# Performance work log

Hardware: AMD Instinct MI355X
Metric: run time of the kernel (lower is better)

Reference implementation:

```python
import jax, jax.numpy as jnp
import numpy as np

B, T, C_IN, C_HID, C_EMB, K, MAX_DUR = 16, 512, 512, 256, 384, 5, 8
MAX_MEL = T * MAX_DUR  # static upper bound on regulated length (4096)
LRELU_SLOPE = 0.3
PAD = (K - 1) // 2
EPS = 1e-5


def setup_inputs() -> dict:
    key = jax.random.key(0)
    ks = jax.random.split(key, 14)
    s = 0.05
    return {
        "x": jax.random.normal(ks[0], (B, T, C_IN), jnp.float32),
        "x_res": jax.random.normal(ks[1], (B, T, C_IN), jnp.float32),
        "duration_target": jax.random.randint(ks[2], (B, T), 0, MAX_DUR, dtype=jnp.int32),
        "embeddings": jax.random.normal(ks[3], (B, T, C_EMB), jnp.float32),
        "src_mask": jnp.zeros((B, T), jnp.bool_),
        "conv1_w": s * jax.random.normal(ks[4], (K, C_IN, C_HID), jnp.float32),
        "conv1_b": jnp.zeros((C_HID,), jnp.float32),
        "ln1_g": jnp.ones((C_HID,), jnp.float32),
        "ln1_b": jnp.zeros((C_HID,), jnp.float32),
        "conv2_w": s * jax.random.normal(ks[5], (K, C_HID, C_HID), jnp.float32),
        "conv2_b": jnp.zeros((C_HID,), jnp.float32),
        "ln2_g": jnp.ones((C_HID,), jnp.float32),
        "ln2_b": jnp.zeros((C_HID,), jnp.float32),
        "lin_w": s * jax.random.normal(ks[6], (C_HID, 1), jnp.float32),
        "lin_b": jnp.zeros((1,), jnp.float32),
    }


def _conv1d(x, w, b):
    # x: [B, T, Cin], w: [K, Cin, Cout] -> [B, T, Cout] (same padding)
    y = jax.lax.conv_general_dilated(
        x, w, window_strides=(1,), padding=[(PAD, PAD)],
        dimension_numbers=("NWC", "WIO", "NWC"))
    return y + b


def _layer_norm(x, g, b):
    mu = jnp.mean(x, axis=-1, keepdims=True)
    var = jnp.mean(jnp.square(x - mu), axis=-1, keepdims=True)
    return (x - mu) * jax.lax.rsqrt(var + EPS) * g + b


def _duration_predictor(x, mask, c1w, c1b, g1, b1, c2w, c2b, g2, b2, lw, lb):
    h = jax.nn.leaky_relu(_conv1d(x, c1w, c1b), LRELU_SLOPE)
    h = _layer_norm(h, g1, b1)  # dropout is identity at eval
    h = jax.nn.leaky_relu(_conv1d(h, c2w, c2b), LRELU_SLOPE)
    h = _layer_norm(h, g2, b2)
    h = (h @ lw + lb).squeeze(-1)  # [B, T]
    return jnp.where(mask, 0.0, h)


def _length_regulate(x, duration):
    # Fused prefix-sum + gather replacement for the looped expand/cat/pad.
    # token i occupies output frames [cumsum[i-1], cumsum[i])
    cum = jnp.cumsum(duration, axis=1)              # [B, T]
    total = cum[:, -1]                              # [B] mel lengths
    pos = jnp.arange(MAX_MEL, dtype=cum.dtype)      # [MAX_MEL]
    idx = jax.vmap(lambda c: jnp.searchsorted(c, pos, side="right"))(cum)  # [B, MAX_MEL]
    idx = jnp.clip(idx, 0, duration.shape[1] - 1)
    valid = (pos[None, :] < total[:, None])         # [B, MAX_MEL]
    out = jnp.take_along_axis(x, idx[..., None], axis=1)
    out = out * valid[..., None].astype(x.dtype)    # zero-padded past mel_len
    return out, total.astype(jnp.int32)


def reference(x, x_res, duration_target, embeddings, src_mask,
              conv1_w, conv1_b, ln1_g, ln1_b, conv2_w, conv2_b, ln2_g, ln2_b,
              lin_w, lin_b):
    # upsample_train path: x_res is detached before the duration predictor
    x_res = jax.lax.stop_gradient(x_res)
    log_duration_prediction = _duration_predictor(
        x_res, src_mask, conv1_w, conv1_b, ln1_g, ln1_b,
        conv2_w, conv2_b, ln2_g, ln2_b, lin_w, lin_b)
    x_up, _ = _length_regulate(x, duration_target)
    emb_up, _ = _length_regulate(embeddings, duration_target)
    return x_up, log_duration_prediction, emb_up
```

## Files before the change

### kernel.cpp

```cpp
#include <hip/hip_runtime.h>


constexpr int Bn = 16, Tn = 512, CIN1 = 512, CHID = 256, CEMB = 384, MAXMEL = 4096;
constexpr int NROWS = Bn * Tn;
#define LRELU 0.3f
#define EPSV 1e-5f

typedef __attribute__((ext_vector_type(8))) short bf16x8;
typedef __attribute__((ext_vector_type(4))) float f32x4;
typedef unsigned short ushort_t;

static __device__ __forceinline__ ushort_t f2bf(float f) {
  unsigned u = __builtin_bit_cast(unsigned, f);
  unsigned r = (u + 0x7fffu + ((u >> 16) & 1u)) >> 16;
  return (ushort_t)r;
}
static __device__ __forceinline__ float bf2f(ushort_t h) {
  unsigned u = ((unsigned)h) << 16;
  return __builtin_bit_cast(float, u);
}

__global__ __launch_bounds__(256) void wprep_kernel(const float* __restrict__ w,
                                                    ushort_t* __restrict__ hi,
                                                    ushort_t* __restrict__ lo,
                                                    int CI) {
  const int gid = blockIdx.x * 256 + threadIdx.x;
  const int ksh = gid / (CI * 256);
  const int rem = gid - ksh * CI * 256;
  const int ci = rem >> 8, co = rem & 255;
  const float v = w[gid];
  const ushort_t h = f2bf(v);
  const int ci32 = ci >> 5, cob = co >> 4;
  const int l = ((ci >> 3) & 3) * 16 + (co & 15);
  const int j = ci & 7;
  const size_t dst = ((size_t)((ksh * (CI / 32) + ci32) * 16 + cob)) * 512 + l * 8 + j;
  hi[dst] = h;
  lo[dst] = f2bf(v - bf2f(h));
}

template <int CI, bool F32IN>
__global__ __launch_bounds__(512, 4) void conv_mfma_kernel(
    const float* __restrict__ xin,
    const ushort_t* __restrict__ inhi,
    const ushort_t* __restrict__ wBhi,
    const ushort_t* __restrict__ wBlo,
    float* __restrict__ part) {
  constexpr int CIQ = CI / 4;
  constexpr int NCHUNK = CIQ / 64;
  constexpr int ROWS = 132, LDSTRIDE = 72;
  __shared__ ushort_t sAhi[ROWS * LDSTRIDE];
  __shared__ ushort_t sAlo[F32IN ? ROWS * LDSTRIDE : 1];

  const int mt = blockIdx.x, ns = blockIdx.y, ks = blockIdx.z;
  const int b = mt >> 2, t0 = (mt & 3) * 128;
  const int tid = threadIdx.x;
  const int l = tid & 63, w = tid >> 6;
  const int mh = w >> 1, nh = w & 1;
  const int lm = l & 15, lq = l >> 4;

  f32x4 acc[2][4];
#pragma unroll
  for (int im = 0; im < 2; ++im)
#pragma unroll
    for (int jn = 0; jn < 4; ++jn) acc[im][jn] = (f32x4){0.f, 0.f, 0.f, 0.f};

  const ushort_t* pBh = wBhi + l * 8;
  const ushort_t* pBl = wBlo + l * 8;
  const int cobBase = ns * 8 + nh * 4;
  const int rowBase = mh * 32 + lm;

#pragma unroll 1
  for (int chunk = 0; chunk < NCHUNK; ++chunk) {
    {
      const int cibase = ks * CIQ + chunk * 64;
#pragma unroll 1
      for (int i = 0; i < 9; ++i) {
        const int p = i * 512 + tid;
        if (p < ROWS * 32) {
          const int r = p >> 5, c2 = (p & 31) * 2;
          const int t = t0 - 2 + r;
          unsigned hv = 0, lv = 0;
          if ((unsigned)t < (unsigned)Tn) {
            const size_t src = (size_t)(b * Tn + t) * CI + cibase + c2;
            if (F32IN) {
              const float2 v = *(const float2*)(xin + src);
              const ushort_t h0 = f2bf(v.x), h1 = f2bf(v.y);
              hv = (unsigned)h0 | ((unsigned)h1 << 16);
              lv = (unsigned)f2bf(v.x - bf2f(h0)) |
                   ((unsigned)f2bf(v.y - bf2f(h1)) << 16);
            } else {
              hv = *(const unsigned*)(inhi + src);
            }
          }
          *(unsigned*)&sAhi[r * LDSTRIDE + c2] = hv;
          if (F32IN) *(unsigned*)&sAlo[r * LDSTRIDE + c2] = lv;
        }
      }
    }
    __syncthreads();

#pragma unroll 1
    for (int ksh = 0; ksh < 5; ++ksh) {
#pragma unroll
      for (int kk = 0; kk < 2; ++kk) {
        bf16x8 a_h[2], a_l[2];
#pragma unroll
        for (int im = 0; im < 2; ++im) {
          const int ad = (rowBase + im * 16 + ksh) * LDSTRIDE + kk * 32 + lq * 8;
          a_h[im] = *(const bf16x8*)&sAhi[ad];
          if (F32IN) a_l[im] = *(const bf16x8*)&sAlo[ad];
        }
        const int ci32 = ks * (CIQ / 32) + chunk * 2 + kk;
        const int frBase = (ksh * (CI / 32) + ci32) * 16 + cobBase;
#pragma unroll
        for (int jn = 0; jn < 4; ++jn) {
          const size_t fo = (size_t)(frBase + jn) * 512;
          const bf16x8 bh = *(const bf16x8*)(pBh + fo);
          const bf16x8 bl = *(const bf16x8*)(pBl + fo);
#pragma unroll
          for (int im = 0; im < 2; ++im) {
            acc[im][jn] = __builtin_amdgcn_mfma_f32_16x16x32_bf16(a_h[im], bh, acc[im][jn], 0, 0, 0);
            if (F32IN)
              acc[im][jn] = __builtin_amdgcn_mfma_f32_16x16x32_bf16(a_l[im], bh, acc[im][jn], 0, 0, 0);
            acc[im][jn] = __builtin_amdgcn_mfma_f32_16x16x32_bf16(a_h[im], bl, acc[im][jn], 0, 0, 0);
          }
        }
      }
    }
    __syncthreads();
  }

  float* pOut = part + (size_t)ks * NROWS * 256;
#pragma unroll
  for (int im = 0; im < 2; ++im)
#pragma unroll
    for (int jn = 0; jn < 4; ++jn) {
      const int col = ns * 128 + nh * 64 + jn * 16 + lm;
#pragma unroll
      for (int reg = 0; reg < 4; ++reg) {
        const int grow = b * Tn + t0 + mh * 32 + im * 16 + lq * 4 + reg;
        pOut[(size_t)grow * 256 + col] = acc[im][jn][reg];
      }
    }
}

template <bool FINAL>
__global__ __launch_bounds__(256) void ln_kernel(
    const float* __restrict__ part,
    const float* __restrict__ bias, const float* __restrict__ g,
    const float* __restrict__ be, ushort_t* __restrict__ h1,
    const float* __restrict__ lw, const float* __restrict__ lb,
    const unsigned char* __restrict__ mask, float* __restrict__ ldp) {
  const int row = blockIdx.x * 4 + (threadIdx.x >> 6);
  const int l = threadIdx.x & 63;
  const float4 bi = ((const float4*)bias)[l];
  float v0 = bi.x, v1 = bi.y, v2 = bi.z, v3 = bi.w;
#pragma unroll
  for (int k = 0; k < 4; ++k) {
    const float4 p = ((const float4*)(part + (size_t)k * NROWS * 256))[row * 64 + l];
    v0 += p.x; v1 += p.y; v2 += p.z; v3 += p.w;
  }
  v0 = (v0 > 0.f) ? v0 : LRELU * v0;
  v1 = (v1 > 0.f) ? v1 : LRELU * v1;
  v2 = (v2 > 0.f) ? v2 : LRELU * v2;
  v3 = (v3 > 0.f) ? v3 : LRELU * v3;
  float s = v0 + v1 + v2 + v3;
  float s2 = v0 * v0 + v1 * v1 + v2 * v2 + v3 * v3;
#pragma unroll
  for (int off = 32; off >= 1; off >>= 1) {
    s += __shfl_xor(s, off);
    s2 += __shfl_xor(s2, off);
  }
  const float mu = s * (1.f / 256.f);
  const float var = s2 * (1.f / 256.f) - mu * mu;
  const float rs = rsqrtf(var + EPSV);
  const float4 gg = ((const float4*)g)[l];
  const float4 bb = ((const float4*)be)[l];
  const float h0 = (v0 - mu) * rs * gg.x + bb.x;
  const float h1v = (v1 - mu) * rs * gg.y + bb.y;
  const float h2 = (v2 - mu) * rs * gg.z + bb.z;
  const float h3 = (v3 - mu) * rs * gg.w + bb.w;
  if (!FINAL) {
    ushort4 uh;
    uh.x = f2bf(h0); uh.y = f2bf(h1v); uh.z = f2bf(h2); uh.w = f2bf(h3);
    ((ushort4*)h1)[row * 64 + l] = uh;
  } else {
    const float4 lv = ((const float4*)lw)[l];
    float d = h0 * lv.x + h1v * lv.y + h2 * lv.z + h3 * lv.w;
#pragma unroll
    for (int off = 32; off >= 1; off >>= 1) d += __shfl_xor(d, off);
    if (l == 0) {
      float val = d + lb[0];
      if (mask[row]) val = 0.f;
      ldp[row] = val;
    }
  }
}

__global__ __launch_bounds__(512) void build_idx_kernel(const int* __restrict__ dur,
                                                        int* __restrict__ idx) {
  __shared__ int cum[Tn];
  const int b = blockIdx.x, t = threadIdx.x;
  const int d = dur[b * Tn + t];
  cum[t] = d;
  __syncthreads();
  for (int off = 1; off < Tn; off <<= 1) {
    int v = (t >= off) ? cum[t - off] : 0;
    __syncthreads();
    cum[t] += v;
    __syncthreads();
  }
  const int end = cum[t];
  for (int p = end - d; p < end; ++p) idx[b * MAXMEL + p] = t;
  const int total = cum[Tn - 1];
  for (int p = total + t; p < MAXMEL; p += Tn) idx[b * MAXMEL + p] = -1;
}

__global__ __launch_bounds__(256) void gather_kernel(const float* __restrict__ x,
                                                     const float* __restrict__ emb,
                                                     const int* __restrict__ idx,
                                                     float* __restrict__ x_up,
                                                     float* __restrict__ emb_up) {
  const float4* x4 = (const float4*)x;
  const float4* e4 = (const float4*)emb;
  float4* xu4 = (float4*)x_up;
  float4* eu4 = (float4*)emb_up;
  const int tid0 = blockIdx.x * 256 + threadIdx.x;
  const int stride = gridDim.x * 256;
  const float4 z = make_float4(0.f, 0.f, 0.f, 0.f);
  for (int u = tid0; u < Bn * MAXMEL * 128; u += stride) {
    const int bp = u >> 7, i = u & 127;
    const int t = idx[bp];
    const int b = bp >> 12;
    xu4[u] = (t >= 0) ? x4[((b << 9) + t) * 128 + i] : z;
  }
  for (int u = tid0; u < Bn * MAXMEL * 96; u += stride) {
    const int bp = u / 96, i = u - bp * 96;
    const int t = idx[bp];
    const int b = bp >> 12;
    eu4[u] = (t >= 0) ? e4[((b << 9) + t) * 96 + i] : z;
  }
}

extern "C" void kernel_launch(void* const* d_in, const int* in_sizes, int n_in,
                              void* d_out, int out_size, void* d_ws, size_t ws_size,
                              hipStream_t stream) {
  const float* x     = (const float*)d_in[0];
  const float* x_res = (const float*)d_in[1];
  const int*   dur   = (const int*)d_in[2];
  const float* emb   = (const float*)d_in[3];
  const unsigned char* mask = (const unsigned char*)d_in[4];
  const float* c1w = (const float*)d_in[5];
  const float* c1b = (const float*)d_in[6];
  const float* g1  = (const float*)d_in[7];
  const float* b1  = (const float*)d_in[8];
  const float* c2w = (const float*)d_in[9];
  const float* c2b = (const float*)d_in[10];
  const float* g2  = (const float*)d_in[11];
  const float* b2  = (const float*)d_in[12];
  const float* lw  = (const float*)d_in[13];
  const float* lb  = (const float*)d_in[14];

  float* x_up   = (float*)d_out;
  float* ldp    = x_up + (size_t)Bn * MAXMEL * CIN1;
  float* emb_up = ldp + (size_t)Bn * Tn;

  float* part = emb_up;
  ushort_t* w1hi = (ushort_t*)(part + (size_t)4 * NROWS * 256);
  ushort_t* w1lo = w1hi + (size_t)5 * 512 * 256;
  ushort_t* w2hi = w1lo + (size_t)5 * 512 * 256;
  ushort_t* w2lo = w2hi + (size_t)5 * 256 * 256;

  int* idx = (int*)d_ws;
  ushort_t* h1 = (ushort_t*)((char*)d_ws + (size_t)Bn * MAXMEL * sizeof(int));

  wprep_kernel<<<5 * 512 * 256 / 256, 256, 0, stream>>>(c1w, w1hi, w1lo, 512);
  wprep_kernel<<<5 * 256 * 256 / 256, 256, 0, stream>>>(c2w, w2hi, w2lo, 256);
  conv_mfma_kernel<512, true><<<dim3(64, 2, 4), 512, 0, stream>>>(
      x_res, nullptr, w1hi, w1lo, part);
  ln_kernel<false><<<NROWS / 4, 256, 0, stream>>>(
      part, c1b, g1, b1, h1, nullptr, nullptr, nullptr, nullptr);
  conv_mfma_kernel<256, false><<<dim3(64, 2, 4), 512, 0, stream>>>(
      nullptr, h1, w2hi, w2lo, part);
  ln_kernel<true><<<NROWS / 4, 256, 0, stream>>>(
      part, c2b, g2, b2, nullptr, lw, lb, mask, ldp);
  build_idx_kernel<<<Bn, Tn, 0, stream>>>(dur, idx);
  gather_kernel<<<2048, 256, 0, stream>>>(x, emb, idx, x_up, emb_up);
}
```

Baseline: 408.5 us.

## Fuse conv with LayerNorm, drop split-bf16 precision, use nontemporal gather stores

Drops the hi/lo bf16 split so each conv needs one MFMA per fragment instead of two or three. LayerNorm and LeakyReLU are fused into the conv kernel through an LDS tile, which removes the split-K partial buffer and the separate LN kernels. Tiles shrink to 32 rows by full 256 columns per block, and the gather stores become nontemporal. The plain-bf16 path risks accuracy relative to the fp32 reference, and the 256-block grid may leave much of the GPU idle during the convs.

Result: no change. 413.6 us (+1.2%).

```diff
diff --git a/kernel.cpp b/kernel.cpp
--- a/kernel.cpp
+++ b/kernel.cpp
@@ -15,47 +15,42 @@
   unsigned r = (u + 0x7fffu + ((u >> 16) & 1u)) >> 16;
   return (ushort_t)r;
 }
-static __device__ __forceinline__ float bf2f(ushort_t h) {
-  unsigned u = ((unsigned)h) << 16;
-  return __builtin_bit_cast(float, u);
-}
 
 __global__ __launch_bounds__(256) void wprep_kernel(const float* __restrict__ w,
                                                     ushort_t* __restrict__ hi,
-                                                    ushort_t* __restrict__ lo,
                                                     int CI) {
   const int gid = blockIdx.x * 256 + threadIdx.x;
   const int ksh = gid / (CI * 256);
   const int rem = gid - ksh * CI * 256;
   const int ci = rem >> 8, co = rem & 255;
-  const float v = w[gid];
-  const ushort_t h = f2bf(v);
   const int ci32 = ci >> 5, cob = co >> 4;
   const int l = ((ci >> 3) & 3) * 16 + (co & 15);
   const int j = ci & 7;
   const size_t dst = ((size_t)((ksh * (CI / 32) + ci32) * 16 + cob)) * 512 + l * 8 + j;
-  hi[dst] = h;
-  lo[dst] = f2bf(v - bf2f(h));
+  hi[dst] = f2bf(w[gid]);
 }
 
 template <int CI, bool F32IN>
-__global__ __launch_bounds__(512, 4) void conv_mfma_kernel(
+__global__ __launch_bounds__(256, 2) void conv_ln_mfma_kernel(
     const float* __restrict__ xin,
-    const ushort_t* __restrict__ inhi,
-    const ushort_t* __restrict__ wBhi,
-    const ushort_t* __restrict__ wBlo,
-    float* __restrict__ part) {
-  constexpr int CIQ = CI / 4;
-  constexpr int NCHUNK = CIQ / 64;
-  constexpr int ROWS = 132, LDSTRIDE = 72;
-  __shared__ ushort_t sAhi[ROWS * LDSTRIDE];
-  __shared__ ushort_t sAlo[F32IN ? ROWS * LDSTRIDE : 1];
-
-  const int mt = blockIdx.x, ns = blockIdx.y, ks = blockIdx.z;
-  const int b = mt >> 2, t0 = (mt & 3) * 128;
+    const ushort_t* __restrict__ inbf,
+    const ushort_t* __restrict__ wB,
+    const float* __restrict__ bias, const float* __restrict__ g,
+    const float* __restrict__ be,
+    ushort_t* __restrict__ h1out,
+    const float* __restrict__ lw, const float* __restrict__ lb,
+    const unsigned char* __restrict__ mask, float* __restrict__ ldp) {
+  constexpr bool FINAL = !F32IN;
+  constexpr int NCHUNK = CI / 64;
+  constexpr int LDSTRIDE = 72;
+  __shared__ ushort_t sA[36 * LDSTRIDE];
+  __shared__ float sC[32 * 260];
+  __shared__ float sps[32 * 8], spq[32 * 8];
+  __shared__ float smu[32], srs[32];
+
+  const int b = blockIdx.x >> 4, t0 = (blockIdx.x & 15) * 32;
   const int tid = threadIdx.x;
-  const int l = tid & 63, w = tid >> 6;
-  const int mh = w >> 1, nh = w & 1;
+  const int l = tid & 63, nh = tid >> 6;
   const int lm = l & 15, lq = l >> 4;
 
   f32x4 acc[2][4];
@@ -64,36 +59,29 @@
 #pragma unroll
     for (int jn = 0; jn < 4; ++jn) acc[im][jn] = (f32x4){0.f, 0.f, 0.f, 0.f};
 
-  const ushort_t* pBh = wBhi + l * 8;
-  const ushort_t* pBl = wBlo + l * 8;
-  const int cobBase = ns * 8 + nh * 4;
-  const int rowBase = mh * 32 + lm;
+  const ushort_t* pB = wB + l * 8;
 
 #pragma unroll 1
   for (int chunk = 0; chunk < NCHUNK; ++chunk) {
     {
-      const int cibase = ks * CIQ + chunk * 64;
+      const int cibase = chunk * 64;
 #pragma unroll 1
-      for (int i = 0; i < 9; ++i) {
-        const int p = i * 512 + tid;
-        if (p < ROWS * 32) {
+      for (int i = 0; i < 5; ++i) {
+        const int p = i * 256 + tid;
+        if (p < 36 * 32) {
           const int r = p >> 5, c2 = (p & 31) * 2;
           const int t = t0 - 2 + r;
-          unsigned hv = 0, lv = 0;
+          unsigned hv = 0;
           if ((unsigned)t < (unsigned)Tn) {
             const size_t src = (size_t)(b * Tn + t) * CI + cibase + c2;
             if (F32IN) {
               const float2 v = *(const float2*)(xin + src);
-              const ushort_t h0 = f2bf(v.x), h1 = f2bf(v.y);
-              hv = (unsigned)h0 | ((unsigned)h1 << 16);
-              lv = (unsigned)f2bf(v.x - bf2f(h0)) |
-                   ((unsigned)f2bf(v.y - bf2f(h1)) << 16);
+              hv = (unsigned)f2bf(v.x) | ((unsigned)f2bf(v.y) << 16);
             } else {
-              hv = *(const unsigned*)(inhi + src);
+              hv = *(const unsigned*)(inbf + src);
             }
           }
-          *(unsigned*)&sAhi[r * LDSTRIDE + c2] = hv;
-          if (F32IN) *(unsigned*)&sAlo[r * LDSTRIDE + c2] = lv;
+          *(unsigned*)&sA[r * LDSTRIDE + c2] = hv;
         }
       }
     }
@@ -103,96 +91,104 @@
     for (int ksh = 0; ksh < 5; ++ksh) {
 #pragma unroll
       for (int kk = 0; kk < 2; ++kk) {
-        bf16x8 a_h[2], a_l[2];
-#pragma unroll
-        for (int im = 0; im < 2; ++im) {
-          const int ad = (rowBase + im * 16 + ksh) * LDSTRIDE + kk * 32 + lq * 8;
-          a_h[im] = *(const bf16x8*)&sAhi[ad];
-          if (F32IN) a_l[im] = *(const bf16x8*)&sAlo[ad];
-        }
-        const int ci32 = ks * (CIQ / 32) + chunk * 2 + kk;
-        const int frBase = (ksh * (CI / 32) + ci32) * 16 + cobBase;
+        bf16x8 a[2];
+#pragma unroll
+        for (int im = 0; im < 2; ++im)
+          a[im] = *(const bf16x8*)&sA[(im * 16 + lm + ksh) * LDSTRIDE + kk * 32 + lq * 8];
+        const int frBase = (ksh * (CI / 32) + chunk * 2 + kk) * 16 + nh * 4;
 #pragma unroll
         for (int jn = 0; jn < 4; ++jn) {
-          const size_t fo = (size_t)(frBase + jn) * 512;
-          const bf16x8 bh = *(const bf16x8*)(pBh + fo);
-          const bf16x8 bl = *(const bf16x8*)(pBl + fo);
-#pragma unroll
-          for (int im = 0; im < 2; ++im) {
-            acc[im][jn] = __builtin_amdgcn_mfma_f32_16x16x32_bf16(a_h[im], bh, acc[im][jn], 0, 0, 0);
-            if (F32IN)
-              acc[im][jn] = __builtin_amdgcn_mfma_f32_16x16x32_bf16(a_l[im], bh, acc[im][jn], 0, 0, 0);
-            acc[im][jn] = __builtin_amdgcn_mfma_f32_16x16x32_bf16(a_h[im], bl, acc[im][jn], 0, 0, 0);
-          }
+          const bf16x8 bv = *(const bf16x8*)(pB + (size_t)(frBase + jn) * 512);
+#pragma unroll
+          for (int im = 0; im < 2; ++im)
+            acc[im][jn] = __builtin_amdgcn_mfma_f32_16x16x32_bf16(a[im], bv, acc[im][jn], 0, 0, 0);
         }
       }
     }
     __syncthreads();
   }
 
-  float* pOut = part + (size_t)ks * NROWS * 256;
 #pragma unroll
   for (int im = 0; im < 2; ++im)
 #pragma unroll
     for (int jn = 0; jn < 4; ++jn) {
-      const int col = ns * 128 + nh * 64 + jn * 16 + lm;
-#pragma unroll
-      for (int reg = 0; reg < 4; ++reg) {
-        const int grow = b * Tn + t0 + mh * 32 + im * 16 + lq * 4 + reg;
-        pOut[(size_t)grow * 256 + col] = acc[im][jn][reg];
-      }
-    }
-}
-
-template <bool FINAL>
-__global__ __launch_bounds__(256) void ln_kernel(
-    const float* __restrict__ part,
-    const float* __restrict__ bias, const float* __restrict__ g,
-    const float* __restrict__ be, ushort_t* __restrict__ h1,
-    const float* __restrict__ lw, const float* __restrict__ lb,
-    const unsigned char* __restrict__ mask, float* __restrict__ ldp) {
-  const int row = blockIdx.x * 4 + (threadIdx.x >> 6);
-  const int l = threadIdx.x & 63;
-  const float4 bi = ((const float4*)bias)[l];
-  float v0 = bi.x, v1 = bi.y, v2 = bi.z, v3 = bi.w;
-#pragma unroll
-  for (int k = 0; k < 4; ++k) {
-    const float4 p = ((const float4*)(part + (size_t)k * NROWS * 256))[row * 64 + l];
-    v0 += p.x; v1 += p.y; v2 += p.z; v3 += p.w;
-  }
-  v0 = (v0 > 0.f) ? v0 : LRELU * v0;
-  v1 = (v1 > 0.f) ? v1 : LRELU * v1;
-  v2 = (v2 > 0.f) ? v2 : LRELU * v2;
-  v3 = (v3 > 0.f) ? v3 : LRELU * v3;
-  float s = v0 + v1 + v2 + v3;
-  float s2 = v0 * v0 + v1 * v1 + v2 * v2 + v3 * v3;
-#pragma unroll
-  for (int off = 32; off >= 1; off >>= 1) {
-    s += __shfl_xor(s, off);
-    s2 += __shfl_xor(s2, off);
-  }
-  const float mu = s * (1.f / 256.f);
-  const float var = s2 * (1.f / 256.f) - mu * mu;
-  const float rs = rsqrtf(var + EPSV);
-  const float4 gg = ((const float4*)g)[l];
-  const float4 bb = ((const float4*)be)[l];
-  const float h0 = (v0 - mu) * rs * gg.x + bb.x;
-  const float h1v = (v1 - mu) * rs * gg.y + bb.y;
-  const float h2 = (v2 - mu) * rs * gg.z + bb.z;
-  const float h3 = (v3 - mu) * rs * gg.w + bb.w;
+      const int col = nh * 64 + jn * 16 + lm;
+#pragma unroll
+      for (int reg = 0; reg < 4; ++reg)
+        sC[(im * 16 + lq * 4 + reg) * 260 + col] = acc[im][jn][reg];
+    }
+  __syncthreads();
+
+  const int row = tid >> 3, sg = tid & 7;
+  float v[32];
+  float s = 0.f, s2 = 0.f;
+#pragma unroll
+  for (int q = 0; q < 8; ++q) {
+    const f32x4 c4 = *(const f32x4*)&sC[row * 260 + sg * 32 + q * 4];
+    const f32x4 b4 = ((const f32x4*)bias)[sg * 8 + q];
+    float x0 = c4.x + b4.x, x1 = c4.y + b4.y, x2 = c4.z + b4.z, x3 = c4.w + b4.w;
+    x0 = (x0 > 0.f) ? x0 : LRELU * x0;
+    x1 = (x1 > 0.f) ? x1 : LRELU * x1;
+    x2 = (x2 > 0.f) ? x2 : LRELU * x2;
+    x3 = (x3 > 0.f) ? x3 : LRELU * x3;
+    v[q * 4] = x0; v[q * 4 + 1] = x1; v[q * 4 + 2] = x2; v[q * 4 + 3] = x3;
+    s += x0 + x1 + x2 + x3;
+    s2 += x0 * x0 + x1 * x1 + x2 * x2 + x3 * x3;
+  }
+  sps[row * 8 + sg] = s;
+  spq[row * 8 + sg] = s2;
+  __syncthreads();
+  if (tid < 32) {
+    float ts = 0.f, tq = 0.f;
+#pragma unroll
+    for (int q = 0; q < 8; ++q) { ts += sps[tid * 8 + q]; tq += spq[tid * 8 + q]; }
+    const float mu = ts * (1.f / 256.f);
+    const float var = tq * (1.f / 256.f) - mu * mu;
+    smu[tid] = mu;
+    srs[tid] = rsqrtf(var + EPSV);
+  }
+  __syncthreads();
+  const float mu = smu[row], rs = srs[row];
+  const int rowg = b * Tn + t0 + row;
+
   if (!FINAL) {
-    ushort4 uh;
-    uh.x = f2bf(h0); uh.y = f2bf(h1v); uh.z = f2bf(h2); uh.w = f2bf(h3);
-    ((ushort4*)h1)[row * 64 + l] = uh;
+    unsigned up[16];
+#pragma unroll
+    for (int q = 0; q < 8; ++q) {
+      const f32x4 g4 = ((const f32x4*)g)[sg * 8 + q];
+      const f32x4 e4 = ((const f32x4*)be)[sg * 8 + q];
+      const float h0 = (v[q * 4] - mu) * rs * g4.x + e4.x;
+      const float h1 = (v[q * 4 + 1] - mu) * rs * g4.y + e4.y;
+      const float h2 = (v[q * 4 + 2] - mu) * rs * g4.z + e4.z;
+      const float h3 = (v[q * 4 + 3] - mu) * rs * g4.w + e4.w;
+      up[q * 2] = (unsigned)f2bf(h0) | ((unsigned)f2bf(h1) << 16);
+      up[q * 2 + 1] = (unsigned)f2bf(h2) | ((unsigned)f2bf(h3) << 16);
+    }
+    uint4* dst = (uint4*)(h1out + (size_t)rowg * 256 + sg * 32);
+#pragma unroll
+    for (int q = 0; q < 4; ++q)
+      dst[q] = make_uint4(up[q * 4], up[q * 4 + 1], up[q * 4 + 2], up[q * 4 + 3]);
   } else {
-    const float4 lv = ((const float4*)lw)[l];
-    float d = h0 * lv.x + h1v * lv.y + h2 * lv.z + h3 * lv.w;
-#pragma unroll
-    for (int off = 32; off >= 1; off >>= 1) d += __shfl_xor(d, off);
-    if (l == 0) {
-      float val = d + lb[0];
-      if (mask[row]) val = 0.f;
-      ldp[row] = val;
+    float d = 0.f;
+#pragma unroll
+    for (int q = 0; q < 8; ++q) {
+      const f32x4 g4 = ((const f32x4*)g)[sg * 8 + q];
+      const f32x4 e4 = ((const f32x4*)be)[sg * 8 + q];
+      const f32x4 l4 = ((const f32x4*)lw)[sg * 8 + q];
+      d += ((v[q * 4] - mu) * rs * g4.x + e4.x) * l4.x;
+      d += ((v[q * 4 + 1] - mu) * rs * g4.y + e4.y) * l4.y;
+      d += ((v[q * 4 + 2] - mu) * rs * g4.z + e4.z) * l4.z;
+      d += ((v[q * 4 + 3] - mu) * rs * g4.w + e4.w) * l4.w;
+    }
+    sps[row * 8 + sg] = d;
+    __syncthreads();
+    if (tid < 32) {
+      float td = 0.f;
+#pragma unroll
+      for (int q = 0; q < 8; ++q) td += sps[tid * 8 + q];
+      float val = td + lb[0];
+      if (mask[b * Tn + t0 + tid]) val = 0.f;
+      ldp[b * Tn + t0 + tid] = val;
     }
   }
 }
@@ -221,24 +217,26 @@
                                                      const int* __restrict__ idx,
                                                      float* __restrict__ x_up,
                                                      float* __restrict__ emb_up) {
-  const float4* x4 = (const float4*)x;
-  const float4* e4 = (const float4*)emb;
-  float4* xu4 = (float4*)x_up;
-  float4* eu4 = (float4*)emb_up;
+  const f32x4* x4 = (const f32x4*)x;
+  const f32x4* e4 = (const f32x4*)emb;
+  f32x4* xu4 = (f32x4*)x_up;
+  f32x4* eu4 = (f32x4*)emb_up;
   const int tid0 = blockIdx.x * 256 + threadIdx.x;
   const int stride = gridDim.x * 256;
-  const float4 z = make_float4(0.f, 0.f, 0.f, 0.f);
+  const f32x4 z = (f32x4){0.f, 0.f, 0.f, 0.f};
   for (int u = tid0; u < Bn * MAXMEL * 128; u += stride) {
     const int bp = u >> 7, i = u & 127;
     const int t = idx[bp];
     const int b = bp >> 12;
-    xu4[u] = (t >= 0) ? x4[((b << 9) + t) * 128 + i] : z;
+    const f32x4 v = (t >= 0) ? x4[((b << 9) + t) * 128 + i] : z;
+    __builtin_nontemporal_store(v, &xu4[u]);
   }
   for (int u = tid0; u < Bn * MAXMEL * 96; u += stride) {
     const int bp = u / 96, i = u - bp * 96;
     const int t = idx[bp];
     const int b = bp >> 12;
-    eu4[u] = (t >= 0) ? e4[((b << 9) + t) * 96 + i] : z;
+    const f32x4 v = (t >= 0) ? e4[((b << 9) + t) * 96 + i] : z;
+    __builtin_nontemporal_store(v, &eu4[u]);
   }
 }
 
@@ -265,25 +263,17 @@
   float* ldp    = x_up + (size_t)Bn * MAXMEL * CIN1;
   float* emb_up = ldp + (size_t)Bn * Tn;
 
-  float* part = emb_up;
-  ushort_t* w1hi = (ushort_t*)(part + (size_t)4 * NROWS * 256);
-  ushort_t* w1lo = w1hi + (size_t)5 * 512 * 256;
-  ushort_t* w2hi = w1lo + (size_t)5 * 512 * 256;
-  ushort_t* w2lo = w2hi + (size_t)5 * 256 * 256;
-
   int* idx = (int*)d_ws;
-  ushort_t* h1 = (ushort_t*)((char*)d_ws + (size_t)Bn * MAXMEL * sizeof(int));
-
-  wprep_kernel<<<5 * 512 * 256 / 256, 256, 0, stream>>>(c1w, w1hi, w1lo, 512);
-  wprep_kernel<<<5 * 256 * 256 / 256, 256, 0, stream>>>(c2w, w2hi, w2lo, 256);
-  conv_mfma_kernel<512, true><<<dim3(64, 2, 4), 512, 0, stream>>>(
-      x_res, nullptr, w1hi, w1lo, part);
-  ln_kernel<false><<<NROWS / 4, 256, 0, stream>>>(
-      part, c1b, g1, b1, h1, nullptr, nullptr, nullptr, nullptr);
-  conv_mfma_kernel<256, false><<<dim3(64, 2, 4), 512, 0, stream>>>(
-      nullptr, h1, w2hi, w2lo, part);
-  ln_kernel<true><<<NROWS / 4, 256, 0, stream>>>(
-      part, c2b, g2, b2, nullptr, lw, lb, mask, ldp);
+  ushort_t* h1 = (ushort_t*)((char*)d_ws + (size_t)Bn * MAXMEL * 4);
+  ushort_t* w1 = h1 + (size_t)NROWS * 256;
+  ushort_t* w2 = w1 + (size_t)5 * 512 * 256;
+
+  wprep_kernel<<<5 * 512 * 256 / 256, 256, 0, stream>>>(c1w, w1, 512);
+  wprep_kernel<<<5 * 256 * 256 / 256, 256, 0, stream>>>(c2w, w2, 256);
   build_idx_kernel<<<Bn, Tn, 0, stream>>>(dur, idx);
+  conv_ln_mfma_kernel<512, true><<<256, 256, 0, stream>>>(
+      x_res, nullptr, w1, c1b, g1, b1, h1, nullptr, nullptr, nullptr, nullptr);
+  conv_ln_mfma_kernel<256, false><<<256, 256, 0, stream>>>(
+      nullptr, h1, w2, c2b, g2, b2, nullptr, lw, lb, mask, ldp);
   gather_kernel<<<2048, 256, 0, stream>>>(x, emb, idx, x_up, emb_up);
 }
```

## Drop split-bf16 conv precision, use 32x32 MFMA tiles without split-K, nontemporal gather stores

Applied to the files above, without the earlier changes.

The conv kernels no longer emulate fp32 with hi/lo bf16 pairs. They use a single bf16 pass with 32x32x16 MFMA, smaller 32-row tiles, no split-K partial buffers, and a swizzled LDS layout. The LayerNorm kernels now read one raw buffer instead of summing four partials. The gather writes use nontemporal stores, and build_idx is launched earlier. This cuts MFMA count and partial-sum traffic, but drops accuracy from roughly fp32 to plain bf16, which may break the tolerance.

After: 371.2 us. -9.1%, faster.

```diff
diff --git a/kernel.cpp b/kernel.cpp
--- a/kernel.cpp
+++ b/kernel.cpp
@@ -8,6 +8,7 @@
 
 typedef __attribute__((ext_vector_type(8))) short bf16x8;
 typedef __attribute__((ext_vector_type(4))) float f32x4;
+typedef __attribute__((ext_vector_type(16))) float f32x16;
 typedef unsigned short ushort_t;
 
 static __device__ __forceinline__ ushort_t f2bf(float f) {
@@ -15,85 +16,66 @@
   unsigned r = (u + 0x7fffu + ((u >> 16) & 1u)) >> 16;
   return (ushort_t)r;
 }
-static __device__ __forceinline__ float bf2f(ushort_t h) {
-  unsigned u = ((unsigned)h) << 16;
-  return __builtin_bit_cast(float, u);
-}
 
 __global__ __launch_bounds__(256) void wprep_kernel(const float* __restrict__ w,
-                                                    ushort_t* __restrict__ hi,
-                                                    ushort_t* __restrict__ lo,
+                                                    ushort_t* __restrict__ out,
                                                     int CI) {
   const int gid = blockIdx.x * 256 + threadIdx.x;
   const int ksh = gid / (CI * 256);
   const int rem = gid - ksh * CI * 256;
   const int ci = rem >> 8, co = rem & 255;
-  const float v = w[gid];
-  const ushort_t h = f2bf(v);
-  const int ci32 = ci >> 5, cob = co >> 4;
-  const int l = ((ci >> 3) & 3) * 16 + (co & 15);
+  const int ci16 = ci >> 4, cob32 = co >> 5;
+  const int l = ((ci >> 3) & 1) * 32 + (co & 31);
   const int j = ci & 7;
-  const size_t dst = ((size_t)((ksh * (CI / 32) + ci32) * 16 + cob)) * 512 + l * 8 + j;
-  hi[dst] = h;
-  lo[dst] = f2bf(v - bf2f(h));
+  const size_t dst = ((size_t)((ksh * (CI / 16) + ci16) * 8 + cob32)) * 512 + l * 8 + j;
+  out[dst] = f2bf(w[gid]);
 }
 
 template <int CI, bool F32IN>
-__global__ __launch_bounds__(512, 4) void conv_mfma_kernel(
+__global__ __launch_bounds__(256, 2) void conv_mfma_kernel(
     const float* __restrict__ xin,
-    const ushort_t* __restrict__ inhi,
-    const ushort_t* __restrict__ wBhi,
-    const ushort_t* __restrict__ wBlo,
-    float* __restrict__ part) {
-  constexpr int CIQ = CI / 4;
-  constexpr int NCHUNK = CIQ / 64;
-  constexpr int ROWS = 132, LDSTRIDE = 72;
-  __shared__ ushort_t sAhi[ROWS * LDSTRIDE];
-  __shared__ ushort_t sAlo[F32IN ? ROWS * LDSTRIDE : 1];
-
-  const int mt = blockIdx.x, ns = blockIdx.y, ks = blockIdx.z;
-  const int b = mt >> 2, t0 = (mt & 3) * 128;
+    const ushort_t* __restrict__ inbf,
+    const ushort_t* __restrict__ wB,
+    float* __restrict__ hraw) {
+  constexpr int NCHUNK = CI / 64;
+  constexpr int ROWS = 36, LDSTRIDE = 72;
+  __shared__ ushort_t sA[ROWS * LDSTRIDE];
+
+  const int mt = blockIdx.x, ns = blockIdx.y;
+  const int b = mt >> 4, t0 = (mt & 15) * 32;
   const int tid = threadIdx.x;
-  const int l = tid & 63, w = tid >> 6;
-  const int mh = w >> 1, nh = w & 1;
-  const int lm = l & 15, lq = l >> 4;
-
-  f32x4 acc[2][4];
-#pragma unroll
-  for (int im = 0; im < 2; ++im)
-#pragma unroll
-    for (int jn = 0; jn < 4; ++jn) acc[im][jn] = (f32x4){0.f, 0.f, 0.f, 0.f};
-
-  const ushort_t* pBh = wBhi + l * 8;
-  const ushort_t* pBl = wBlo + l * 8;
-  const int cobBase = ns * 8 + nh * 4;
-  const int rowBase = mh * 32 + lm;
+  const int l = tid & 63, nh = tid >> 6;
+  const int lm = l & 31, lq = l >> 5;
+  const int cob32 = ns * 4 + nh;
+
+  f32x16 acc;
+#pragma unroll
+  for (int i = 0; i < 16; ++i) acc[i] = 0.f;
+
+  const ushort_t* pB = wB + (size_t)cob32 * 512 + l * 8;
 
 #pragma unroll 1
   for (int chunk = 0; chunk < NCHUNK; ++chunk) {
     {
-      const int cibase = ks * CIQ + chunk * 64;
+      const int cibase = chunk * 64;
 #pragma unroll 1
-      for (int i = 0; i < 9; ++i) {
-        const int p = i * 512 + tid;
+      for (int i = 0; i < 5; ++i) {
+        const int p = i * 256 + tid;
         if (p < ROWS * 32) {
           const int r = p >> 5, c2 = (p & 31) * 2;
           const int t = t0 - 2 + r;
-          unsigned hv = 0, lv = 0;
+          unsigned hv = 0;
           if ((unsigned)t < (unsigned)Tn) {
             const size_t src = (size_t)(b * Tn + t) * CI + cibase + c2;
             if (F32IN) {
               const float2 v = *(const float2*)(xin + src);
-              const ushort_t h0 = f2bf(v.x), h1 = f2bf(v.y);
-              hv = (unsigned)h0 | ((unsigned)h1 << 16);
-              lv = (unsigned)f2bf(v.x - bf2f(h0)) |
-                   ((unsigned)f2bf(v.y - bf2f(h1)) << 16);
+              hv = (unsigned)f2bf(v.x) | ((unsigned)f2bf(v.y) << 16);
             } else {
-              hv = *(const unsigned*)(inhi + src);
+              hv = *(const unsigned*)(inbf + src);
             }
           }
-          *(unsigned*)&sAhi[r * LDSTRIDE + c2] = hv;
-          if (F32IN) *(unsigned*)&sAlo[r * LDSTRIDE + c2] = lv;
+          const int sw = ((r >> 3) & 3) << 3;
+          *(unsigned*)&sA[r * LDSTRIDE + (c2 ^ sw)] = hv;
         }
       }
     }
@@ -101,65 +83,41 @@
 
 #pragma unroll 1
     for (int ksh = 0; ksh < 5; ++ksh) {
-#pragma unroll
-      for (int kk = 0; kk < 2; ++kk) {
-        bf16x8 a_h[2], a_l[2];
-#pragma unroll
-        for (int im = 0; im < 2; ++im) {
-          const int ad = (rowBase + im * 16 + ksh) * LDSTRIDE + kk * 32 + lq * 8;
-          a_h[im] = *(const bf16x8*)&sAhi[ad];
-          if (F32IN) a_l[im] = *(const bf16x8*)&sAlo[ad];
-        }
-        const int ci32 = ks * (CIQ / 32) + chunk * 2 + kk;
-        const int frBase = (ksh * (CI / 32) + ci32) * 16 + cobBase;
-#pragma unroll
-        for (int jn = 0; jn < 4; ++jn) {
-          const size_t fo = (size_t)(frBase + jn) * 512;
-          const bf16x8 bh = *(const bf16x8*)(pBh + fo);
-          const bf16x8 bl = *(const bf16x8*)(pBl + fo);
-#pragma unroll
-          for (int im = 0; im < 2; ++im) {
-            acc[im][jn] = __builtin_amdgcn_mfma_f32_16x16x32_bf16(a_h[im], bh, acc[im][jn], 0, 0, 0);
-            if (F32IN)
-              acc[im][jn] = __builtin_amdgcn_mfma_f32_16x16x32_bf16(a_l[im], bh, acc[im][jn], 0, 0, 0);
-            acc[im][jn] = __builtin_amdgcn_mfma_f32_16x16x32_bf16(a_h[im], bl, acc[im][jn], 0, 0, 0);
-          }
-        }
+      const int r = lm + ksh;
+      const int sw = ((r >> 3) & 3) << 3;
+      const size_t bbase = (size_t)((ksh * (CI / 16) + chunk * 4) * 8) * 512;
+#pragma unroll
+      for (int kk = 0; kk < 4; ++kk) {
+        const int c = (kk * 16 + lq * 8) ^ sw;
+        const bf16x8 a = *(const bf16x8*)&sA[r * LDSTRIDE + c];
+        const bf16x8 bv = *(const bf16x8*)(pB + bbase + (size_t)kk * 8 * 512);
+        acc = __builtin_amdgcn_mfma_f32_32x32x16_bf16(a, bv, acc, 0, 0, 0);
       }
     }
     __syncthreads();
   }
 
-  float* pOut = part + (size_t)ks * NROWS * 256;
-#pragma unroll
-  for (int im = 0; im < 2; ++im)
-#pragma unroll
-    for (int jn = 0; jn < 4; ++jn) {
-      const int col = ns * 128 + nh * 64 + jn * 16 + lm;
-#pragma unroll
-      for (int reg = 0; reg < 4; ++reg) {
-        const int grow = b * Tn + t0 + mh * 32 + im * 16 + lq * 4 + reg;
-        pOut[(size_t)grow * 256 + col] = acc[im][jn][reg];
-      }
-    }
+  const int col = ns * 128 + nh * 32 + lm;
+  float* pOut = hraw + (size_t)(b * Tn + t0) * 256 + col;
+#pragma unroll
+  for (int reg = 0; reg < 16; ++reg) {
+    const int row = (reg & 3) + 8 * (reg >> 2) + 4 * lq;
+    pOut[(size_t)row * 256] = acc[reg];
+  }
 }
 
 template <bool FINAL>
 __global__ __launch_bounds__(256) void ln_kernel(
-    const float* __restrict__ part,
+    const float* __restrict__ hraw,
     const float* __restrict__ bias, const float* __restrict__ g,
     const float* __restrict__ be, ushort_t* __restrict__ h1,
     const float* __restrict__ lw, const float* __restrict__ lb,
     const unsigned char* __restrict__ mask, float* __restrict__ ldp) {
   const int row = blockIdx.x * 4 + (threadIdx.x >> 6);
   const int l = threadIdx.x & 63;
-  const float4 bi = ((const float4*)bias)[l];
-  float v0 = bi.x, v1 = bi.y, v2 = bi.z, v3 = bi.w;
-#pragma unroll
-  for (int k = 0; k < 4; ++k) {
-    const float4 p = ((const float4*)(part + (size_t)k * NROWS * 256))[row * 64 + l];
-    v0 += p.x; v1 += p.y; v2 += p.z; v3 += p.w;
-  }
+  const f32x4 p = ((const f32x4*)hraw)[row * 64 + l];
+  const f32x4 bi = ((const f32x4*)bias)[l];
+  float v0 = p.x + bi.x, v1 = p.y + bi.y, v2 = p.z + bi.z, v3 = p.w + bi.w;
   v0 = (v0 > 0.f) ? v0 : LRELU * v0;
   v1 = (v1 > 0.f) ? v1 : LRELU * v1;
   v2 = (v2 > 0.f) ? v2 : LRELU * v2;
@@ -174,8 +132,8 @@
   const float mu = s * (1.f / 256.f);
   const float var = s2 * (1.f / 256.f) - mu * mu;
   const float rs = rsqrtf(var + EPSV);
-  const float4 gg = ((const float4*)g)[l];
-  const float4 bb = ((const float4*)be)[l];
+  const f32x4 gg = ((const f32x4*)g)[l];
+  const f32x4 bb = ((const f32x4*)be)[l];
   const float h0 = (v0 - mu) * rs * gg.x + bb.x;
   const float h1v = (v1 - mu) * rs * gg.y + bb.y;
   const float h2 = (v2 - mu) * rs * gg.z + bb.z;
@@ -185,7 +143,7 @@
     uh.x = f2bf(h0); uh.y = f2bf(h1v); uh.z = f2bf(h2); uh.w = f2bf(h3);
     ((ushort4*)h1)[row * 64 + l] = uh;
   } else {
-    const float4 lv = ((const float4*)lw)[l];
+    const f32x4 lv = ((const f32x4*)lw)[l];
     float d = h0 * lv.x + h1v * lv.y + h2 * lv.z + h3 * lv.w;
 #pragma unroll
     for (int off = 32; off >= 1; off >>= 1) d += __shfl_xor(d, off);
@@ -221,24 +179,26 @@
                                                      const int* __restrict__ idx,
                                                      float* __restrict__ x_up,
                                                      float* __restrict__ emb_up) {
-  const float4* x4 = (const float4*)x;
-  const float4* e4 = (const float4*)emb;
-  float4* xu4 = (float4*)x_up;
-  float4* eu4 = (float4*)emb_up;
+  const f32x4* x4 = (const f32x4*)x;
+  const f32x4* e4 = (const f32x4*)emb;
+  f32x4* xu4 = (f32x4*)x_up;
+  f32x4* eu4 = (f32x4*)emb_up;
   const int tid0 = blockIdx.x * 256 + threadIdx.x;
   const int stride = gridDim.x * 256;
-  const float4 z = make_float4(0.f, 0.f, 0.f, 0.f);
+  const f32x4 z = (f32x4){0.f, 0.f, 0.f, 0.f};
   for (int u = tid0; u < Bn * MAXMEL * 128; u += stride) {
     const int bp = u >> 7, i = u & 127;
     const int t = idx[bp];
     const int b = bp >> 12;
-    xu4[u] = (t >= 0) ? x4[((b << 9) + t) * 128 + i] : z;
+    const f32x4 v = (t >= 0) ? x4[((b << 9) + t) * 128 + i] : z;
+    __builtin_nontemporal_store(v, &xu4[u]);
   }
   for (int u = tid0; u < Bn * MAXMEL * 96; u += stride) {
     const int bp = u / 96, i = u - bp * 96;
     const int t = idx[bp];
     const int b = bp >> 12;
-    eu4[u] = (t >= 0) ? e4[((b << 9) + t) * 96 + i] : z;
+    const f32x4 v = (t >= 0) ? e4[((b << 9) + t) * 96 + i] : z;
+    __builtin_nontemporal_store(v, &eu4[u]);
   }
 }
 
@@ -265,25 +225,23 @@
   float* ldp    = x_up + (size_t)Bn * MAXMEL * CIN1;
   float* emb_up = ldp + (size_t)Bn * Tn;
 
-  float* part = emb_up;
-  ushort_t* w1hi = (ushort_t*)(part + (size_t)4 * NROWS * 256);
-  ushort_t* w1lo = w1hi + (size_t)5 * 512 * 256;
-  ushort_t* w2hi = w1lo + (size_t)5 * 512 * 256;
-  ushort_t* w2lo = w2hi + (size_t)5 * 256 * 256;
+  float* hraw = emb_up;
 
   int* idx = (int*)d_ws;
-  ushort_t* h1 = (ushort_t*)((char*)d_ws + (size_t)Bn * MAXMEL * sizeof(int));
-
-  wprep_kernel<<<5 * 512 * 256 / 256, 256, 0, stream>>>(c1w, w1hi, w1lo, 512);
-  wprep_kernel<<<5 * 256 * 256 / 256, 256, 0, stream>>>(c2w, w2hi, w2lo, 256);
-  conv_mfma_kernel<512, true><<<dim3(64, 2, 4), 512, 0, stream>>>(
-      x_res, nullptr, w1hi, w1lo, part);
+  ushort_t* h1 = (ushort_t*)((char*)d_ws + (size_t)Bn * MAXMEL * 4);
+  ushort_t* w1 = h1 + (size_t)NROWS * 256;
+  ushort_t* w2 = w1 + (size_t)5 * 512 * 256;
+
+  wprep_kernel<<<5 * 512 * 256 / 256, 256, 0, stream>>>(c1w, w1, 512);
+  wprep_kernel<<<5 * 256 * 256 / 256, 256, 0, stream>>>(c2w, w2, 256);
+  build_idx_kernel<<<Bn, Tn, 0, stream>>>(dur, idx);
+  conv_mfma_kernel<512, true><<<dim3(256, 2), 256, 0, stream>>>(
+      x_res, nullptr, w1, hraw);
   ln_kernel<false><<<NROWS / 4, 256, 0, stream>>>(
-      part, c1b, g1, b1, h1, nullptr, nullptr, nullptr, nullptr);
-  conv_mfma_kernel<256, false><<<dim3(64, 2, 4), 512, 0, stream>>>(
-      nullptr, h1, w2hi, w2lo, part);
+      hraw, c1b, g1, b1, h1, nullptr, nullptr, nullptr, nullptr);
+  conv_mfma_kernel<256, false><<<dim3(256, 2), 256, 0, stream>>>(
+      nullptr, h1, w2, hraw);
   ln_kernel<true><<<NROWS / 4, 256, 0, stream>>>(
-      part, c2b, g2, b2, nullptr, lw, lb, mask, ldp);
-  build_idx_kernel<<<Bn, Tn, 0, stream>>>(dur, idx);
+      hraw, c2b, g2, b2, nullptr, lw, lb, mask, ldp);
   gather_kernel<<<2048, 256, 0, stream>>>(x, emb, idx, x_up, emb_up);
 }
```
